# Kernel tuning notes

Hardware: AMD Instinct MI355X
Metric: run time of the kernel (lower is better)

## Reference

```python
import jax, jax.numpy as jnp
import numpy as np

N_NODES = 50000
N_EDGES = 800000
B, W, D, OUT = 2, 128, 64, 128


def setup_inputs() -> dict:
    key = jax.random.key(0)
    ks = jax.random.split(key, 8)
    s = lambda k, shape, fan: jax.random.normal(k, shape, dtype=jnp.float32) / np.sqrt(fan)
    return {
        "x": jax.random.normal(ks[0], (B, N_NODES, W), dtype=jnp.float32),
        "embeddings": jax.random.normal(ks[1], (N_NODES, D), dtype=jnp.float32),
        "edge_index": jax.random.randint(ks[2], (2, N_EDGES), 0, N_NODES, dtype=jnp.int64),
        "Wq": s(ks[3], (D, D), D),
        "Wk": s(ks[4], (D, D), D),
        "v": s(ks[5], (D,), D),
        "fcW": s(ks[6], (OUT, 2 * W), 2 * W),
        "fcb": jnp.zeros((OUT,), dtype=jnp.float32),
    }


def reference(x, embeddings, edge_index, Wq, Wk, v, fcW, fcb):
    B_, N, W_ = x.shape
    src, dst = edge_index[0], edge_index[1]

    # Project once on nodes, then gather per edge (same math as gather-then-linear).
    e_q = embeddings @ Wq.T        # [N, D]
    e_k = embeddings @ Wk.T        # [N, D]
    score = jnp.tanh(e_q[src] + e_k[dst]) @ v   # [E]

    # Scatter-softmax over destination nodes.
    max_vals = jax.ops.segment_max(score, dst, num_segments=N)   # [N], -inf for empty
    exp_src = jnp.exp(score - max_vals[dst])                     # [E]
    sum_exp = jax.ops.segment_sum(exp_src, dst, num_segments=N)  # [N]
    attn = exp_src / (sum_exp[dst] + 1e-8)                       # [E]

    # Weighted scatter-add aggregation of source features.
    weighted = x[:, src, :] * attn[None, :, None]                # [B, E, W]
    agg = jax.ops.segment_sum(jnp.swapaxes(weighted, 0, 1), dst, num_segments=N)  # [N, B, W]
    agg = jnp.swapaxes(agg, 0, 1)                                # [B, N, W]

    out = jnp.concatenate([x, agg], axis=-1) @ fcW.T + fcb       # [B, N, OUT]
    return jax.nn.relu(out)
```

## Files before the change

### kernel.cpp

```cpp
#include <hip/hip_runtime.h>
#include <hip/hip_bf16.h>
#include <math.h>

#define N_NODES 50000
#define N_EDGES 800000
#define BB 2
#define WFEAT 128
#define DD 64
#define OUTD 128
#define NROWS (BB * N_NODES)
#define SCAN_B 256
#define NBLK ((N_NODES + SCAN_B - 1) / SCAN_B)

#define PROJ_TB ((N_NODES + 127) / 128)
#define CVTX_B 6250
#define CVTW_B 16
#define HIST_B 3125
#define TRIPLE_B (3 * HIST_B)
#define PREP_B (TRIPLE_B + CVTW_B)
#define PS_B (PROJ_TB + NBLK)

#define RECB 384

typedef __attribute__((ext_vector_type(8))) short bf16x8;
typedef __attribute__((ext_vector_type(4))) float f32x4;
typedef __attribute__((ext_vector_type(2))) float f32x2;
typedef __attribute__((ext_vector_type(8))) unsigned short ushort8;

#define PRESCALE 2.8853900817779268f
#define L2E 1.4426950408889634f

static __device__ __forceinline__ unsigned short f2bf(float f) {
    __hip_bfloat16 h = __float2bfloat16(f);
    return *reinterpret_cast<unsigned short*>(&h);
}
static __device__ __forceinline__ float bf_lo(unsigned int w) {
    return __uint_as_float(w << 16);
}
static __device__ __forceinline__ float bf_hi(unsigned int w) {
    return __uint_as_float(w & 0xFFFF0000u);
}
static __device__ __forceinline__ float exp2_hw(float x) {
    float r;
    asm("v_exp_f32 %0, %1" : "=v"(r) : "v"(x));
    return r;
}
template <int CTRL>
static __device__ __forceinline__ float ror_add(float x) {
    int xi = __float_as_int(x);
    int r = __builtin_amdgcn_update_dpp(xi, xi, CTRL, 0xF, 0xF, true);
    return x + __int_as_float(r);
}
static __device__ __forceinline__ float row_reduce(float x) {
    x = ror_add<0x128>(x);
    x = ror_add<0x124>(x);
    x = ror_add<0x122>(x);
    x = ror_add<0x121>(x);
    return x;
}

__global__ __launch_bounds__(256) void prep_kernel(const float* __restrict__ x,
                                                   unsigned short* __restrict__ xb2,
                                                   unsigned char* __restrict__ nrec,
                                                   const float* __restrict__ fcW,
                                                   unsigned short* __restrict__ fcWb,
                                                   const int* __restrict__ dstp,
                                                   int* __restrict__ deg,
                                                   unsigned short* __restrict__ posin) {
    int bid = blockIdx.x;
    int tid = threadIdx.x;
    if (bid < TRIPLE_B) {
        int q = bid / 3;
        int r = bid - q * 3;
        if (r < 2) {
            int t = (q * 2 + r) * 256 + tid;
            const float4* in4 = (const float4*)x;
            float4 a = in4[2 * t], b = in4[2 * t + 1];
            ushort8 o;
            o[0] = f2bf(a.x); o[1] = f2bf(a.y); o[2] = f2bf(a.z); o[3] = f2bf(a.w);
            o[4] = f2bf(b.x); o[5] = f2bf(b.y); o[6] = f2bf(b.z); o[7] = f2bf(b.w);
            int f0 = t * 8;
            int bb = f0 >= N_NODES * WFEAT;
            int rem = f0 - bb * (N_NODES * WFEAT);
            int node = rem >> 7, feat = rem & 127;
            *reinterpret_cast<ushort8*>(&xb2[(size_t)node * 256 + bb * 128 + feat]) = o;
            int w0 = __builtin_amdgcn_cvt_pk_fp8_f32(a.x, a.y, 0, false);
            w0     = __builtin_amdgcn_cvt_pk_fp8_f32(a.z, a.w, w0, true);
            int w1 = __builtin_amdgcn_cvt_pk_fp8_f32(b.x, b.y, 0, false);
            w1     = __builtin_amdgcn_cvt_pk_fp8_f32(b.z, b.w, w1, true);
            uint2 pk; pk.x = (unsigned int)w0; pk.y = (unsigned int)w1;
            *reinterpret_cast<uint2*>(&nrec[(size_t)node * RECB + 128 + bb * 128 + feat]) = pk;
        } else {
            int e = q * 256 + tid;
            int d = dstp[e];
            posin[e] = (unsigned short)atomicAdd(&deg[d], 1);
        }
    } else {
        int t = (bid - TRIPLE_B) * 256 + tid;
        const float4* in4 = (const float4*)fcW;
        float4 a = in4[2 * t], b = in4[2 * t + 1];
        ushort8 o;
        o[0] = f2bf(a.x); o[1] = f2bf(a.y); o[2] = f2bf(a.z); o[3] = f2bf(a.w);
        o[4] = f2bf(b.x); o[5] = f2bf(b.y); o[6] = f2bf(b.z); o[7] = f2bf(b.w);
        *reinterpret_cast<ushort8*>(&fcWb[8 * t]) = o;
    }
}

__global__ __launch_bounds__(256) void proj_scan(const float* __restrict__ emb,
                                                 const float* __restrict__ Wq,
                                                 const float* __restrict__ Wk,
                                                 unsigned char* __restrict__ nrec,
                                                 unsigned short* __restrict__ ekb,
                                                 const int* __restrict__ deg,
                                                 int* __restrict__ bsum) {
    __shared__ unsigned short As[128 * 64];
    __shared__ unsigned short Bs[128 * 64];
    int tid = threadIdx.x;
    if (blockIdx.x >= PROJ_TB) {
        int* sh = (int*)As;
        int i = (blockIdx.x - PROJ_TB) * SCAN_B + tid;
        sh[tid] = (i < N_NODES) ? deg[i] : 0;
        __syncthreads();
        for (int s = SCAN_B / 2; s; s >>= 1) {
            if (tid < s) sh[tid] += sh[tid + s];
            __syncthreads();
        }
        if (tid == 0) bsum[blockIdx.x - PROJ_TB] = sh[0];
        return;
    }
    int wave = tid >> 6, lane = tid & 63;
    int wm = wave >> 1, wn = wave & 1;
    int row0 = blockIdx.x * 128;

#pragma unroll
    for (int c = 0; c < 4; ++c) {
        int idx = (c * 256 + tid) * 8;
        int r = idx >> 6, k = idx & 63;
        int byte = (r * 128 + k * 2) ^ ((r & 7) << 4);

        int node = row0 + r;
        ushort8 o = {};
        if (node < N_NODES) {
            const float4* p = (const float4*)(emb + (size_t)node * DD + k);
            float4 a = p[0], b = p[1];
            o[0] = f2bf(a.x); o[1] = f2bf(a.y); o[2] = f2bf(a.z); o[3] = f2bf(a.w);
            o[4] = f2bf(b.x); o[5] = f2bf(b.y); o[6] = f2bf(b.z); o[7] = f2bf(b.w);
        }
        *reinterpret_cast<ushort8*>(reinterpret_cast<char*>(As) + byte) = o;

        const float* wsrc = (r < 64) ? (Wq + r * DD + k) : (Wk + (r - 64) * DD + k);
        float4 wa = *(const float4*)wsrc, wb = *((const float4*)wsrc + 1);
        ushort8 ow;
        ow[0] = f2bf(wa.x); ow[1] = f2bf(wa.y); ow[2] = f2bf(wa.z); ow[3] = f2bf(wa.w);
        ow[4] = f2bf(wb.x); ow[5] = f2bf(wb.y); ow[6] = f2bf(wb.z); ow[7] = f2bf(wb.w);
        *reinterpret_cast<ushort8*>(reinterpret_cast<char*>(Bs) + byte) = ow;
    }
    __syncthreads();

    f32x4 acc[4][4] = {};
#pragma unroll
    for (int kk = 0; kk < 2; ++kk) {
        bf16x8 a[4], b[4];
#pragma unroll
        for (int m = 0; m < 4; ++m) {
            int r = wm * 64 + m * 16 + (lane & 15);
            int k = kk * 32 + (lane >> 4) * 8;
            int byte = (r * 128 + k * 2) ^ ((r & 7) << 4);
            a[m] = *reinterpret_cast<bf16x8*>(reinterpret_cast<char*>(As) + byte);
        }
#pragma unroll
        for (int n = 0; n < 4; ++n) {
            int cn = wn * 64 + n * 16 + (lane & 15);
            int k = kk * 32 + (lane >> 4) * 8;
            int byte = (cn * 128 + k * 2) ^ ((cn & 7) << 4);
            b[n] = *reinterpret_cast<bf16x8*>(reinterpret_cast<char*>(Bs) + byte);
        }
#pragma unroll
        for (int m = 0; m < 4; ++m)
#pragma unroll
            for (int n = 0; n < 4; ++n)
                acc[m][n] = __builtin_amdgcn_mfma_f32_16x16x32_bf16(a[m], b[n], acc[m][n], 0, 0, 0);
    }

#pragma unroll
    for (int m = 0; m < 4; ++m) {
#pragma unroll
        for (int n = 0; n < 4; ++n) {
            int col = wn * 64 + n * 16 + (lane & 15);
#pragma unroll
            for (int j = 0; j < 4; ++j) {
                int row = row0 + wm * 64 + m * 16 + (lane >> 4) * 4 + j;
                if (row < N_NODES) {
                    unsigned short val = f2bf(PRESCALE * acc[m][n][j]);
                    if (col < 64)
                        *reinterpret_cast<unsigned short*>(&nrec[(size_t)row * RECB + col * 2]) = val;
                    else
                        ekb[(size_t)row * DD + col - 64] = val;
                }
            }
        }
    }
}

__global__ void scan_final(const int* __restrict__ deg, const int* __restrict__ bsum,
                           int* __restrict__ rowptr) {
    __shared__ int shb[SCAN_B];
    __shared__ int sh[SCAN_B];
    int tid = threadIdx.x;
    int bv = (tid < NBLK) ? bsum[tid] : 0;
    shb[tid] = bv;
    __syncthreads();
    for (int s = 1; s < SCAN_B; s <<= 1) {
        int t = (tid >= s) ? shb[tid - s] : 0;
        __syncthreads();
        shb[tid] += t;
        __syncthreads();
    }
    int myprefix = (blockIdx.x == 0) ? 0 : shb[blockIdx.x - 1];

    int i = blockIdx.x * SCAN_B + tid;
    int v = (i < N_NODES) ? deg[i] : 0;
    sh[tid] = v;
    __syncthreads();
    for (int s = 1; s < SCAN_B; s <<= 1) {
        int t = 0;
        if (tid >= s) t = sh[tid - s];
        __syncthreads();
        sh[tid] += t;
        __syncthreads();
    }
    if (i < N_NODES) {
        int excl = sh[tid] - v + myprefix;
        rowptr[i] = excl;
        if (i == N_NODES - 1) rowptr[N_NODES] = excl + v;
    }
}

__global__ void scatter_kernel(const int* __restrict__ src, const int* __restrict__ dst,
                               const int* __restrict__ rowptr,
                               const unsigned short* __restrict__ posin,
                               int* __restrict__ src_sorted) {
    int t = blockIdx.x * blockDim.x + threadIdx.x;
    if (t < 12) src_sorted[N_EDGES + t] = 0;
    int e4 = t * 4;
    if (e4 + 3 < N_EDGES) {
        int4 d4 = *reinterpret_cast<const int4*>(dst + e4);
        ushort4 p4 = *reinterpret_cast<const ushort4*>(posin + e4);
        int4 s4 = *reinterpret_cast<const int4*>(src + e4);
        src_sorted[rowptr[d4.x] + p4.x] = s4.x;
        src_sorted[rowptr[d4.y] + p4.y] = s4.y;
        src_sorted[rowptr[d4.z] + p4.z] = s4.z;
        src_sorted[rowptr[d4.w] + p4.w] = s4.w;
    } else {
        for (int e = e4; e < N_EDGES; ++e)
            src_sorted[rowptr[dst[e]] + posin[e]] = src[e];
    }
}

__global__ __launch_bounds__(256) void agg_fused(const unsigned char* __restrict__ nrec,
                                                 const unsigned short* __restrict__ ekb,
                                                 const float* __restrict__ v,
                                                 const int* __restrict__ rowptr,
                                                 const int* __restrict__ src_sorted,
                                                 unsigned short* __restrict__ aggb2) {
    int node = (blockIdx.x * 256 + threadIdx.x) >> 6;
    if (node >= N_NODES) return;
    int lane = threadIdx.x & 63;
    int g = lane >> 4, hl = lane & 15;

    uint2 eku = *reinterpret_cast<const uint2*>(ekb + (size_t)node * DD + 4 * hl);
    f32x2 kk01, kk23;
    kk01.x = bf_lo(eku.x); kk01.y = bf_hi(eku.x);
    kk23.x = bf_lo(eku.y); kk23.y = bf_hi(eku.y);
    float4 vv = *reinterpret_cast<const float4*>(v + 4 * hl);
    f32x2 vv01, vv23;
    vv01.x = vv.x; vv01.y = vv.y; vv23.x = vv.z; vv23.y = vv.w;
    float vs = row_reduce(vv.x + vv.y + vv.z + vv.w);
    float vtotl2 = vs * L2E;
    f32x2 one2; one2.x = 1.f; one2.y = 1.f;

    int beg = rowptr[node], end = rowptr[node + 1];
    int nIter = (end - beg + 3) >> 2;

    float sum = 0.f;
    f32x2 a0[4] = {}, a1[4] = {};

    int s_cur = src_sorted[beg + g];
    int s_nxt = src_sorted[beg + 4 + g];
    const unsigned char* rec = nrec + (unsigned int)(s_cur * RECB + 8 * hl);
    uint2 equ = *reinterpret_cast<const uint2*>(rec);
    uint2 u0 = *reinterpret_cast<const uint2*>(rec + 128);
    uint2 u1 = *reinterpret_cast<const uint2*>(rec + 256);

    for (int i = 0; i < nIter; ++i) {
        bool valid = (beg + 4 * i + g) < end;
        int s_n2 = src_sorted[beg + 4 * (i + 2) + g];
        const unsigned char* recn = nrec + (unsigned int)(s_nxt * RECB + 8 * hl);
        uint2 equn = *reinterpret_cast<const uint2*>(recn);
        uint2 u0n = *reinterpret_cast<const uint2*>(recn + 128);
        uint2 u1n = *reinterpret_cast<const uint2*>(recn + 256);

        f32x2 q01, q23;
        q01.x = bf_lo(equ.x); q01.y = bf_hi(equ.x);
        q23.x = bf_lo(equ.y); q23.y = bf_hi(equ.y);
        q01 += kk01; q23 += kk23;
        f32x2 ex01, ex23;
        ex01.x = exp2_hw(q01.x); ex01.y = exp2_hw(q01.y);
        ex23.x = exp2_hw(q23.x); ex23.y = exp2_hw(q23.y);
        ex01 += one2; ex23 += one2;
        f32x2 rc;
        rc.x = __builtin_amdgcn_rcpf(ex01.x); rc.y = __builtin_amdgcn_rcpf(ex01.y);
        f32x2 r2 = vv01 * rc;
        rc.x = __builtin_amdgcn_rcpf(ex23.x); rc.y = __builtin_amdgcn_rcpf(ex23.y);
        r2 += vv23 * rc;
        float r = row_reduce(r2.x + r2.y);
        float w = exp2_hw(fmaf(-2.f * L2E, r, vtotl2));
        w = valid ? w : 0.f;
        sum += w;

        f32x2 p;
        p = __builtin_amdgcn_cvt_pk_f32_fp8((int)u0.x, false); a0[0] += w * p;
        p = __builtin_amdgcn_cvt_pk_f32_fp8((int)u0.x, true);  a0[1] += w * p;
        p = __builtin_amdgcn_cvt_pk_f32_fp8((int)u0.y, false); a0[2] += w * p;
        p = __builtin_amdgcn_cvt_pk_f32_fp8((int)u0.y, true);  a0[3] += w * p;
        p = __builtin_amdgcn_cvt_pk_f32_fp8((int)u1.x, false); a1[0] += w * p;
        p = __builtin_amdgcn_cvt_pk_f32_fp8((int)u1.x, true);  a1[1] += w * p;
        p = __builtin_amdgcn_cvt_pk_f32_fp8((int)u1.y, false); a1[2] += w * p;
        p = __builtin_amdgcn_cvt_pk_f32_fp8((int)u1.y, true);  a1[3] += w * p;

        equ = equn; u0 = u0n; u1 = u1n;
        s_nxt = s_n2;
    }

    sum += __shfl_xor(sum, 16); sum += __shfl_xor(sum, 32);
#pragma unroll
    for (int j = 0; j < 4; ++j) {
        a0[j].x += __shfl_xor(a0[j].x, 16); a0[j].x += __shfl_xor(a0[j].x, 32);
        a0[j].y += __shfl_xor(a0[j].y, 16); a0[j].y += __shfl_xor(a0[j].y, 32);
        a1[j].x += __shfl_xor(a1[j].x, 16); a1[j].x += __shfl_xor(a1[j].x, 32);
        a1[j].y += __shfl_xor(a1[j].y, 16); a1[j].y += __shfl_xor(a1[j].y, 32);
    }
    float inv = __builtin_amdgcn_rcpf(sum + 1e-8f);

    if (g < 2) {
        float c0 = (g ? a1[0].x : a0[0].x) * inv, c1 = (g ? a1[0].y : a0[0].y) * inv;
        float c2 = (g ? a1[1].x : a0[1].x) * inv, c3 = (g ? a1[1].y : a0[1].y) * inv;
        float c4 = (g ? a1[2].x : a0[2].x) * inv, c5 = (g ? a1[2].y : a0[2].y) * inv;
        float c6 = (g ? a1[3].x : a0[3].x) * inv, c7 = (g ? a1[3].y : a0[3].y) * inv;
        uint4 o;
        o.x = (unsigned int)f2bf(c0) | ((unsigned int)f2bf(c1) << 16);
        o.y = (unsigned int)f2bf(c2) | ((unsigned int)f2bf(c3) << 16);
        o.z = (unsigned int)f2bf(c4) | ((unsigned int)f2bf(c5) << 16);
        o.w = (unsigned int)f2bf(c6) | ((unsigned int)f2bf(c7) << 16);
        *reinterpret_cast<uint4*>(&aggb2[(size_t)node * 256 + (size_t)g * 128 + 8 * hl]) = o;
    }
}

__global__ __launch_bounds__(256) void fc_mfma(const unsigned short* __restrict__ xb2,
                                               const unsigned short* __restrict__ aggb2,
                                               const unsigned short* __restrict__ fcWb,
                                               const float* __restrict__ fcb,
                                               float* __restrict__ out) {
    __shared__ unsigned short As[128 * 64];
    __shared__ unsigned short Bs[128 * 64];
    int tid = threadIdx.x;
    int wave = tid >> 6, lane = tid & 63;
    int wm = wave >> 1, wn = wave & 1;
    int row0 = blockIdx.x * 128;

    f32x4 acc[4][4] = {};

    for (int ks = 0; ks < 4; ++ks) {
        const unsigned short* Asrc = (ks < 2) ? xb2 : aggb2;
        int kbase = (ks & 1) * 64;
        __syncthreads();
#pragma unroll
        for (int c = 0; c < 4; ++c) {
            int idx = (c * 256 + tid) * 8;
            int r = idx >> 6, k = idx & 63;
            int row = row0 + r;
            ulonglong2 val = make_ulonglong2(0ull, 0ull);
            if (row < NROWS) {
                int batch = row >= N_NODES;
                int nd = row - (batch ? N_NODES : 0);
                val = *reinterpret_cast<const ulonglong2*>(
                        &Asrc[(size_t)nd * 256 + batch * 128 + kbase + k]);
            }
            int byte = (r * 128 + k * 2) ^ ((r & 7) << 4);
            *reinterpret_cast<ulonglong2*>(reinterpret_cast<char*>(As) + byte) = val;

            ulonglong2 wv = *reinterpret_cast<const ulonglong2*>(&fcWb[(size_t)r * 256 + ks * 64 + k]);
            *reinterpret_cast<ulonglong2*>(reinterpret_cast<char*>(Bs) + byte) = wv;
        }
        __syncthreads();
#pragma unroll
        for (int kk = 0; kk < 2; ++kk) {
            bf16x8 a[4], b[4];
#pragma unroll
            for (int m = 0; m < 4; ++m) {
                int r = wm * 64 + m * 16 + (lane & 15);
                int k = kk * 32 + (lane >> 4) * 8;
                int byte = (r * 128 + k * 2) ^ ((r & 7) << 4);
                a[m] = *reinterpret_cast<bf16x8*>(reinterpret_cast<char*>(As) + byte);
            }
#pragma unroll
            for (int n = 0; n < 4; ++n) {
                int cn = wn * 64 + n * 16 + (lane & 15);
                int k = kk * 32 + (lane >> 4) * 8;
                int byte = (cn * 128 + k * 2) ^ ((cn & 7) << 4);
                b[n] = *reinterpret_cast<bf16x8*>(reinterpret_cast<char*>(Bs) + byte);
            }
#pragma unroll
            for (int m = 0; m < 4; ++m)
#pragma unroll
                for (int n = 0; n < 4; ++n)
                    acc[m][n] = __builtin_amdgcn_mfma_f32_16x16x32_bf16(a[m], b[n], acc[m][n], 0, 0, 0);
        }
    }
#pragma unroll
    for (int m = 0; m < 4; ++m) {
#pragma unroll
        for (int n = 0; n < 4; ++n) {
            int col = wn * 64 + n * 16 + (lane & 15);
            float bias = fcb[col];
#pragma unroll
            for (int j = 0; j < 4; ++j) {
                int row = row0 + wm * 64 + m * 16 + (lane >> 4) * 4 + j;
                if (row < NROWS)
                    out[(size_t)row * OUTD + col] = fmaxf(acc[m][n][j] + bias, 0.f);
            }
        }
    }
}

extern "C" void kernel_launch(void* const* d_in, const int* in_sizes, int n_in,
                              void* d_out, int out_size, void* d_ws, size_t ws_size,
                              hipStream_t stream) {
    const float* x    = (const float*)d_in[0];
    const float* emb  = (const float*)d_in[1];
    const int*   eidx = (const int*)d_in[2];
    const float* Wq   = (const float*)d_in[3];
    const float* Wk   = (const float*)d_in[4];
    const float* v    = (const float*)d_in[5];
    const float* fcW  = (const float*)d_in[6];
    const float* fcb  = (const float*)d_in[7];
    float* out = (float*)d_out;

    char* ws = (char*)d_ws;
    unsigned char*  nrec = (unsigned char*)ws;                   ws += (size_t)N_NODES * RECB;
    unsigned short* ekb  = (unsigned short*)ws;                  ws += (size_t)N_NODES * DD * 2;
    unsigned short* xb2  = (unsigned short*)ws;                  ws += (size_t)NROWS * WFEAT * 2;
    unsigned short* aggb2= (unsigned short*)ws;                  ws += (size_t)NROWS * WFEAT * 2;
    unsigned short* fcWb = (unsigned short*)ws;                  ws += (size_t)OUTD * 256 * 2;
    int* deg        = (int*)ws;                                  ws += (size_t)N_NODES * 4;
    int* rowptr     = (int*)ws;                                  ws += (size_t)(N_NODES + 1) * 4 + 12;
    unsigned short* posin = (unsigned short*)ws;                 ws += (size_t)N_EDGES * 2;
    int* bsum       = (int*)ws;                                  ws += 256 * 4;
    int* src_sorted = (int*)ws;

    const int* srcp = eidx;
    const int* dstp = eidx + N_EDGES;

    hipMemsetAsync(deg, 0, (size_t)N_NODES * sizeof(int), stream);

    prep_kernel<<<PREP_B, 256, 0, stream>>>(x, xb2, nrec, fcW, fcWb, dstp, deg, posin);
    proj_scan<<<PS_B, 256, 0, stream>>>(emb, Wq, Wk, nrec, ekb, deg, bsum);
    scan_final<<<NBLK, SCAN_B, 0, stream>>>(deg, bsum, rowptr);
    scatter_kernel<<<(N_EDGES / 4 + 255) / 256, 256, 0, stream>>>(srcp, dstp, rowptr, posin,
                                                                  src_sorted);
    agg_fused<<<(N_NODES * 64 + 255) / 256, 256, 0, stream>>>(nrec, ekb, v, rowptr,
                                                              src_sorted, aggb2);
    fc_mfma<<<(NROWS + 127) / 128, 256, 0, stream>>>(xb2, aggb2, fcWb, fcb, out);
}
```

Measured before the change: 154.3 us.

## Fold node projection into prep kernel as per-wave register MFMA blocks

```diff
diff --git a/kernel.cpp b/kernel.cpp
--- a/kernel.cpp
+++ b/kernel.cpp
@@ -12,13 +12,13 @@
 #define SCAN_B 256
 #define NBLK ((N_NODES + SCAN_B - 1) / SCAN_B)
 
-#define PROJ_TB ((N_NODES + 127) / 128)
 #define CVTX_B 6250
 #define CVTW_B 16
 #define HIST_B 3125
 #define TRIPLE_B (3 * HIST_B)
-#define PREP_B (TRIPLE_B + CVTW_B)
-#define PS_B (PROJ_TB + NBLK)
+#define PROJ_W  (N_NODES / 16)
+#define PROJ2_B ((PROJ_W + 3) / 4)
+#define PREP_B (TRIPLE_B + PROJ2_B + CVTW_B)
 
 #define RECB 384
 
@@ -57,6 +57,14 @@
     x = ror_add<0x122>(x);
     x = ror_add<0x121>(x);
     return x;
+}
+static __device__ __forceinline__ bf16x8 pack_bf8(const float* p) {
+    float4 a = *reinterpret_cast<const float4*>(p);
+    float4 b = *reinterpret_cast<const float4*>(p + 4);
+    ushort8 o;
+    o[0] = f2bf(a.x); o[1] = f2bf(a.y); o[2] = f2bf(a.z); o[3] = f2bf(a.w);
+    o[4] = f2bf(b.x); o[5] = f2bf(b.y); o[6] = f2bf(b.z); o[7] = f2bf(b.w);
+    return *reinterpret_cast<bf16x8*>(&o);
 }
 
 __global__ __launch_bounds__(256) void prep_kernel(const float* __restrict__ x,
@@ -66,7 +74,11 @@
                                                    unsigned short* __restrict__ fcWb,
                                                    const int* __restrict__ dstp,
                                                    int* __restrict__ deg,
-                                                   unsigned short* __restrict__ posin) {
+                                                   unsigned short* __restrict__ posin,
+                                                   const float* __restrict__ emb,
+                                                   const float* __restrict__ Wq,
+                                                   const float* __restrict__ Wk,
+                                                   unsigned short* __restrict__ ekb) {
     int bid = blockIdx.x;
     int tid = threadIdx.x;
     if (bid < TRIPLE_B) {
@@ -95,8 +107,35 @@
             int d = dstp[e];
             posin[e] = (unsigned short)atomicAdd(&deg[d], 1);
         }
+    } else if (bid < TRIPLE_B + PROJ2_B) {
+        int wid = (bid - TRIPLE_B) * 4 + (tid >> 6);
+        if (wid >= PROJ_W) return;
+        int lane = tid & 63;
+        int arow = wid * 16 + (lane & 15);
+        int koff = (lane >> 4) * 8;
+        bf16x8 afr0 = pack_bf8(emb + (size_t)arow * DD + koff);
+        bf16x8 afr1 = pack_bf8(emb + (size_t)arow * DD + 32 + koff);
+        int orow = wid * 16 + (lane >> 4) * 4;
+#pragma unroll
+        for (int n = 0; n < 8; ++n) {
+            int wrow = n * 16 + (lane & 15);
+            const float* wp = (n < 4) ? (Wq + (size_t)wrow * DD)
+                                      : (Wk + (size_t)(wrow - 64) * DD);
+            f32x4 acc = {};
+            acc = __builtin_amdgcn_mfma_f32_16x16x32_bf16(afr0, pack_bf8(wp + koff), acc, 0, 0, 0);
+            acc = __builtin_amdgcn_mfma_f32_16x16x32_bf16(afr1, pack_bf8(wp + 32 + koff), acc, 0, 0, 0);
+            int col = n * 16 + (lane & 15);
+#pragma unroll
+            for (int j = 0; j < 4; ++j) {
+                unsigned short val = f2bf(PRESCALE * acc[j]);
+                if (n < 4)
+                    *reinterpret_cast<unsigned short*>(&nrec[(size_t)(orow + j) * RECB + col * 2]) = val;
+                else
+                    ekb[(size_t)(orow + j) * DD + col - 64] = val;
+            }
+        }
     } else {
-        int t = (bid - TRIPLE_B) * 256 + tid;
+        int t = (bid - TRIPLE_B - PROJ2_B) * 256 + tid;
         const float4* in4 = (const float4*)fcW;
         float4 a = in4[2 * t], b = in4[2 * t + 1];
         ushort8 o;
@@ -106,100 +145,16 @@
     }
 }
 
-__global__ __launch_bounds__(256) void proj_scan(const float* __restrict__ emb,
-                                                 const float* __restrict__ Wq,
-                                                 const float* __restrict__ Wk,
-                                                 unsigned char* __restrict__ nrec,
-                                                 unsigned short* __restrict__ ekb,
-                                                 const int* __restrict__ deg,
-                                                 int* __restrict__ bsum) {
-    __shared__ unsigned short As[128 * 64];
-    __shared__ unsigned short Bs[128 * 64];
-    int tid = threadIdx.x;
-    if (blockIdx.x >= PROJ_TB) {
-        int* sh = (int*)As;
-        int i = (blockIdx.x - PROJ_TB) * SCAN_B + tid;
-        sh[tid] = (i < N_NODES) ? deg[i] : 0;
-        __syncthreads();
-        for (int s = SCAN_B / 2; s; s >>= 1) {
-            if (tid < s) sh[tid] += sh[tid + s];
-            __syncthreads();
-        }
-        if (tid == 0) bsum[blockIdx.x - PROJ_TB] = sh[0];
-        return;
-    }
-    int wave = tid >> 6, lane = tid & 63;
-    int wm = wave >> 1, wn = wave & 1;
-    int row0 = blockIdx.x * 128;
-
-#pragma unroll
-    for (int c = 0; c < 4; ++c) {
-        int idx = (c * 256 + tid) * 8;
-        int r = idx >> 6, k = idx & 63;
-        int byte = (r * 128 + k * 2) ^ ((r & 7) << 4);
-
-        int node = row0 + r;
-        ushort8 o = {};
-        if (node < N_NODES) {
-            const float4* p = (const float4*)(emb + (size_t)node * DD + k);
-            float4 a = p[0], b = p[1];
-            o[0] = f2bf(a.x); o[1] = f2bf(a.y); o[2] = f2bf(a.z); o[3] = f2bf(a.w);
-            o[4] = f2bf(b.x); o[5] = f2bf(b.y); o[6] = f2bf(b.z); o[7] = f2bf(b.w);
-        }
-        *reinterpret_cast<ushort8*>(reinterpret_cast<char*>(As) + byte) = o;
-
-        const float* wsrc = (r < 64) ? (Wq + r * DD + k) : (Wk + (r - 64) * DD + k);
-        float4 wa = *(const float4*)wsrc, wb = *((const float4*)wsrc + 1);
-        ushort8 ow;
-        ow[0] = f2bf(wa.x); ow[1] = f2bf(wa.y); ow[2] = f2bf(wa.z); ow[3] = f2bf(wa.w);
-        ow[4] = f2bf(wb.x); ow[5] = f2bf(wb.y); ow[6] = f2bf(wb.z); ow[7] = f2bf(wb.w);
-        *reinterpret_cast<ushort8*>(reinterpret_cast<char*>(Bs) + byte) = ow;
-    }
+__global__ void scan_reduce(const int* __restrict__ deg, int* __restrict__ bsum) {
+    __shared__ int sh[SCAN_B];
+    int i = blockIdx.x * SCAN_B + threadIdx.x;
+    sh[threadIdx.x] = (i < N_NODES) ? deg[i] : 0;
     __syncthreads();
-
-    f32x4 acc[4][4] = {};
-#pragma unroll
-    for (int kk = 0; kk < 2; ++kk) {
-        bf16x8 a[4], b[4];
-#pragma unroll
-        for (int m = 0; m < 4; ++m) {
-            int r = wm * 64 + m * 16 + (lane & 15);
-            int k = kk * 32 + (lane >> 4) * 8;
-            int byte = (r * 128 + k * 2) ^ ((r & 7) << 4);
-            a[m] = *reinterpret_cast<bf16x8*>(reinterpret_cast<char*>(As) + byte);
-        }
-#pragma unroll
-        for (int n = 0; n < 4; ++n) {
-            int cn = wn * 64 + n * 16 + (lane & 15);
-            int k = kk * 32 + (lane >> 4) * 8;
-            int byte = (cn * 128 + k * 2) ^ ((cn & 7) << 4);
-            b[n] = *reinterpret_cast<bf16x8*>(reinterpret_cast<char*>(Bs) + byte);
-        }
-#pragma unroll
-        for (int m = 0; m < 4; ++m)
-#pragma unroll
-            for (int n = 0; n < 4; ++n)
-                acc[m][n] = __builtin_amdgcn_mfma_f32_16x16x32_bf16(a[m], b[n], acc[m][n], 0, 0, 0);
-    }
-
-#pragma unroll
-    for (int m = 0; m < 4; ++m) {
-#pragma unroll
-        for (int n = 0; n < 4; ++n) {
-            int col = wn * 64 + n * 16 + (lane & 15);
-#pragma unroll
-            for (int j = 0; j < 4; ++j) {
-                int row = row0 + wm * 64 + m * 16 + (lane >> 4) * 4 + j;
-                if (row < N_NODES) {
-                    unsigned short val = f2bf(PRESCALE * acc[m][n][j]);
-                    if (col < 64)
-                        *reinterpret_cast<unsigned short*>(&nrec[(size_t)row * RECB + col * 2]) = val;
-                    else
-                        ekb[(size_t)row * DD + col - 64] = val;
-                }
-            }
-        }
-    }
+    for (int s = SCAN_B / 2; s; s >>= 1) {
+        if (threadIdx.x < s) sh[threadIdx.x] += sh[threadIdx.x + s];
+        __syncthreads();
+    }
+    if (threadIdx.x == 0) bsum[blockIdx.x] = sh[0];
 }
 
 __global__ void scan_final(const int* __restrict__ deg, const int* __restrict__ bsum,
@@ -463,8 +418,9 @@
 
     hipMemsetAsync(deg, 0, (size_t)N_NODES * sizeof(int), stream);
 
-    prep_kernel<<<PREP_B, 256, 0, stream>>>(x, xb2, nrec, fcW, fcWb, dstp, deg, posin);
-    proj_scan<<<PS_B, 256, 0, stream>>>(emb, Wq, Wk, nrec, ekb, deg, bsum);
+    prep_kernel<<<PREP_B, 256, 0, stream>>>(x, xb2, nrec, fcW, fcWb, dstp, deg, posin,
+                                            emb, Wq, Wk, ekb);
+    scan_reduce<<<NBLK, SCAN_B, 0, stream>>>(deg, bsum);
     scan_final<<<NBLK, SCAN_B, 0, stream>>>(deg, bsum, rowptr);
     scatter_kernel<<<(N_EDGES / 4 + 255) / 256, 256, 0, stream>>>(srcp, dstp, rowptr, posin,
                                                                   src_sorted);
```

Result: slower. 173.0 us (+12.1%).
